# Kernel optimization log

Hardware: AMD Instinct MI355X
Metric: run time of the kernel (lower is better)

Reference implementation:

```python
import jax, jax.numpy as jnp
import numpy as np

NOTE_RES = 64  # global constant in the original repo; equals D of rep


def _down(x):
    # conv1d with kernel [0.5, 0.5], stride 2 over last axis (even length)
    return 0.5 * (x[..., ::2] + x[..., 1::2])


def setup_inputs() -> dict:
    key = jax.random.key(0)
    k1, k2, k3 = jax.random.split(key, 3)
    B, D, T = 32, NOTE_RES, 4096
    rep = jax.random.normal(k1, (B, D, T), dtype=jnp.float32)
    duration_mask = jax.random.uniform(k2, (B, D, T), dtype=jnp.float32)
    position_mask = jax.random.uniform(k3, (B, D, T), dtype=jnp.float32)
    return {
        "rep": rep,
        "duration_mask": duration_mask,
        "position_mask": position_mask,
        "low_duration": 1,
        "up_duration": 64,
    }


def reference(rep, duration_mask, position_mask, low_duration, up_duration):
    B, D, T = rep.shape  # D == NOTE_RES
    x = jnp.transpose(rep, (0, 2, 1))  # [B, T, NOTE_RES]; conv axis is last
    densed = _down(x)                  # [B, T, NOTE_RES//2]
    pot = NOTE_RES // 2
    res = jnp.zeros((B, T), dtype=rep.dtype)
    for i in range(0, NOTE_RES - low_duration):
        win_len = NOTE_RES - i - 1
        if win_len == pot:
            # descend one pyramid level
            x = densed
            densed = _down(x) if i < NOTE_RES - 2 else None
            d = x  # [B, T, win_len]
            pot //= 2
        else:
            pad_len = win_len - pot
            # mix fine-resolution prefix with coarse suffix -> length win_len
            d = jnp.concatenate([x[..., : 2 * pad_len], densed[..., pad_len:]], axis=-1)
        if win_len < up_duration:
            # sum_w d[b,t,w] * position_mask[b,w,t], gated by duration_mask[b,win_len-1,t]
            contrib = duration_mask[:, win_len - 1, :] * jnp.einsum(
                "btw,bwt->bt", d, position_mask[:, :win_len, :]
            )
            res = res + contrib
    return res[:, None, :]  # [B, 1, T]
```

## Files before the change

### kernel.cpp

```cpp
#include <hip/hip_runtime.h>


#define TT 4096

__device__ __forceinline__ void async_load16(const float* g, float* l) {
  __builtin_amdgcn_global_load_lds(
      (const __attribute__((address_space(1))) void*)g,
      (__attribute__((address_space(3))) void*)l, 16, 0, 0);
}

template <int K0>
__device__ __forceinline__ float roleK(const float* __restrict__ lrep,
                                       const float* __restrict__ lpm,
                                       const float* __restrict__ ldm, int lane,
                                       int low, int up) {
  constexpr int PADN = (K0 + 8 < 32) ? (K0 + 8) : 32;
  constexpr int PMN = (2 * K0 + 14 < 62 ? 2 * K0 + 14 : 62) - K0 + 1;
  float xa[8];
#pragma unroll
  for (int i = 0; i < 8; ++i)
    xa[i] = 0.5f * (lrep[(2 * (K0 + i)) * 64 + lane] +
                    lrep[(2 * (K0 + i) + 1) * 64 + lane]);
  float pmv[PMN];
#pragma unroll
  for (int r = 0; r < PMN; ++r) pmv[r] = lpm[(K0 + r) * 64 + lane];
  float res = 0.f;
#pragma unroll
  for (int pad = 0; pad < PADN; ++pad) {
    const int L = 32 + pad;
    const int kk0 = (pad > K0) ? pad : K0;
    float s = 0.f;
#pragma unroll
    for (int k = kk0; k < K0 + 8; ++k)
      s = fmaf(xa[k - K0], pmv[k + pad - K0], s);
    if (L >= low && L < up) res = fmaf(ldm[(31 + pad) * 64 + lane], s, res);
  }
  return res;
}

__device__ __forceinline__ float role3(const float* __restrict__ lrep,
                                       const float* __restrict__ lpm,
                                       const float* __restrict__ ldm, int lane,
                                       int low, int up) {
  float pmv[31];
#pragma unroll
  for (int r = 0; r < 31; ++r) pmv[r] = lpm[r * 64 + lane];
  float x1[32];
#pragma unroll
  for (int j = 0; j < 32; ++j)
    x1[j] = 0.5f * (lrep[(2 * j) * 64 + lane] + lrep[(2 * j + 1) * 64 + lane]);
  float res = 0.f;
#pragma unroll
  for (int pad = 0; pad < 8; ++pad) {
    const int L = 32 + pad;
    float s = 0.f;
#pragma unroll
    for (int k = pad; k < 8; ++k) s = fmaf(x1[k], pmv[k + pad], s);
    if (L >= low && L < up) res = fmaf(ldm[(31 + pad) * 64 + lane], s, res);
  }
  float x2[16], q1[16];
#pragma unroll
  for (int j = 0; j < 16; ++j) {
    const float a = x1[2 * j], b = x1[2 * j + 1];
    x2[j] = 0.5f * (a + b);
    q1[j] = a * pmv[2 * j] + b * pmv[2 * j + 1];
  }
  float p = 0.f;
#pragma unroll
  for (int pad = 0; pad < 16; ++pad) {
    const int L = 16 + pad;
    float s = p;
#pragma unroll
    for (int k = pad; k < 16; ++k) s = fmaf(x2[k], pmv[k + pad], s);
    if (L >= low && L < up) res = fmaf(ldm[(15 + pad) * 64 + lane], s, res);
    p += q1[pad];
  }
  return res;
}

__device__ __forceinline__ float role4(const float* __restrict__ lrep,
                                       const float* __restrict__ lpm,
                                       const float* __restrict__ ldm, int lane,
                                       int low, int up) {
  float res = 0.f, p = 0.f;
#pragma unroll
  for (int pad = 1; pad < 32; ++pad) {
    const int j = pad - 1;
    const float a = lrep[(2 * j) * 64 + lane];
    const float b = lrep[(2 * j + 1) * 64 + lane];
    const float pa = lpm[(2 * j) * 64 + lane];
    const float pb = lpm[(2 * j + 1) * 64 + lane];
    p = fmaf(a, pa, fmaf(b, pb, p));
    const int L = 32 + pad;
    if (L >= low && L < up) res = fmaf(ldm[(31 + pad) * 64 + lane], p, res);
  }
  return res;
}

template <int M>
__device__ __forceinline__ void level_step(const float* pmv,
                                           const float* __restrict__ ldm,
                                           int lane, int low, int up, float* xf,
                                           float* xc, float& res) {
  float q[M];
#pragma unroll
  for (int j = 0; j < M; ++j) {
    const float a = xf[2 * j], b = xf[2 * j + 1];
    xc[j] = 0.5f * (a + b);
    q[j] = a * pmv[2 * j] + b * pmv[2 * j + 1];
  }
  float p = 0.f;
#pragma unroll
  for (int pad = 0; pad < M; ++pad) {
    const int L = M + pad;
    float s = p;
#pragma unroll
    for (int k = pad; k < M; ++k) s = fmaf(xc[k], pmv[k + pad], s);
    if (L >= low && L < up) res = fmaf(ldm[(M - 1 + pad) * 64 + lane], s, res);
    p += q[pad];
  }
}

__device__ __forceinline__ float role5(const float* __restrict__ lrep,
                                       const float* __restrict__ lpm,
                                       const float* __restrict__ ldm, int lane,
                                       int low, int up) {
  float pmv[15];
#pragma unroll
  for (int r = 0; r < 15; ++r) pmv[r] = lpm[r * 64 + lane];
  float x1[32];
#pragma unroll
  for (int j = 0; j < 32; ++j)
    x1[j] = 0.5f * (lrep[(2 * j) * 64 + lane] + lrep[(2 * j + 1) * 64 + lane]);
  float x2[16];
#pragma unroll
  for (int j = 0; j < 16; ++j) x2[j] = 0.5f * (x1[2 * j] + x1[2 * j + 1]);
  float res = 0.f;
  float x3[8], x4[4], x5[2], x6[1];
  level_step<8>(pmv, ldm, lane, low, up, x2, x3, res);
  level_step<4>(pmv, ldm, lane, low, up, x3, x4, res);
  level_step<2>(pmv, ldm, lane, low, up, x4, x5, res);
  level_step<1>(pmv, ldm, lane, low, up, x5, x6, res);
  return res;
}

__global__ __launch_bounds__(384, 3) void ContextGenerator_34875134444049_kernel(
    const float* __restrict__ rep, const float* __restrict__ dm,
    const float* __restrict__ pm, const int* __restrict__ lowp,
    const int* __restrict__ upp, float* __restrict__ out) {
  __shared__ float lds[192 * 64 + 6 * 64];
  const int wid = threadIdx.x >> 6;
  const int lane = threadIdx.x & 63;
  const int b = blockIdx.x >> 6;
  const int t0 = (blockIdx.x & 63) << 6;
  const size_t base = (size_t)b * 64 * TT + (size_t)t0;

  const size_t lv = (size_t)(lane >> 4) * TT + (size_t)((lane & 15) << 2);
  for (int g = wid; g < 48; g += 6) {
    const float* tbase = (g < 16) ? rep + base
                       : (g < 32) ? pm + base - (size_t)64 * TT
                                  : dm + base - (size_t)128 * TT;
    const float* src = tbase + (size_t)(g << 2) * TT + lv;
    async_load16(src, &lds[g * 256]);
  }

  const int low = lowp[0];
  const int up = upp[0];

  __syncthreads();

  const float* lrep = lds;
  const float* lpm = lds + 64 * 64;
  const float* ldm = lds + 128 * 64;
  float* part = lds + 192 * 64;

  float res;
  if (wid == 0)
    res = roleK<24>(lrep, lpm, ldm, lane, low, up);
  else if (wid == 1)
    res = roleK<16>(lrep, lpm, ldm, lane, low, up);
  else if (wid == 2)
    res = roleK<8>(lrep, lpm, ldm, lane, low, up);
  else if (wid == 3)
    res = role3(lrep, lpm, ldm, lane, low, up);
  else if (wid == 4)
    res = role4(lrep, lpm, ldm, lane, low, up);
  else
    res = role5(lrep, lpm, ldm, lane, low, up);

  if (wid > 0) part[wid * 64 + lane] = res;
  __syncthreads();
  if (wid == 0)
    out[(size_t)b * TT + t0 + lane] = res + part[64 + lane] + part[128 + lane] +
                                      part[192 + lane] + part[256 + lane] +
                                      part[320 + lane];
}

extern "C" void kernel_launch(void* const* d_in, const int* in_sizes, int n_in,
                              void* d_out, int out_size, void* d_ws,
                              size_t ws_size, hipStream_t stream) {
  const float* rep = (const float*)d_in[0];
  const float* dm = (const float*)d_in[1];
  const float* pm = (const float*)d_in[2];
  const int* lowp = (const int*)d_in[3];
  const int* upp = (const int*)d_in[4];
  float* out = (float*)d_out;

  const int blocks = out_size / 64;
  ContextGenerator_34875134444049_kernel<<<blocks, 384, 0, stream>>>(
      rep, dm, pm, lowp, upp, out);
}
```

Measured before the change: 125.7 us.

## Process eight time chunks per block with double-buffered async LDS staging

```diff
diff --git a/kernel.cpp b/kernel.cpp
--- a/kernel.cpp
+++ b/kernel.cpp
@@ -2,11 +2,26 @@
 
 
 #define TT 4096
+#define SL (192 * 64)
 
 __device__ __forceinline__ void async_load16(const float* g, float* l) {
   __builtin_amdgcn_global_load_lds(
       (const __attribute__((address_space(1))) void*)g,
       (__attribute__((address_space(3))) void*)l, 16, 0, 0);
+}
+
+__device__ __forceinline__ void stage(const float* __restrict__ rep,
+                                      const float* __restrict__ dm,
+                                      const float* __restrict__ pm, size_t base,
+                                      float* buf, int wid, int lane) {
+  const size_t lv = (size_t)(lane >> 4) * TT + (size_t)((lane & 15) << 2);
+  for (int g = wid; g < 48; g += 6) {
+    const float* tbase = (g < 16) ? rep + base
+                       : (g < 32) ? pm + base - (size_t)64 * TT
+                                  : dm + base - (size_t)128 * TT;
+    const float* src = tbase + (size_t)(g << 2) * TT + lv;
+    async_load16(src, &buf[g * 256]);
+  }
 }
 
 template <int K0>
@@ -144,56 +159,53 @@
   return res;
 }
 
-__global__ __launch_bounds__(384, 3) void ContextGenerator_34875134444049_kernel(
+__device__ __forceinline__ float compute_role(const float* __restrict__ buf,
+                                              int wid, int lane, int low,
+                                              int up) {
+  const float* lrep = buf;
+  const float* lpm = buf + 64 * 64;
+  const float* ldm = buf + 128 * 64;
+  if (wid == 0) return roleK<24>(lrep, lpm, ldm, lane, low, up);
+  if (wid == 1) return roleK<16>(lrep, lpm, ldm, lane, low, up);
+  if (wid == 2) return roleK<8>(lrep, lpm, ldm, lane, low, up);
+  if (wid == 3) return role3(lrep, lpm, ldm, lane, low, up);
+  if (wid == 4) return role4(lrep, lpm, ldm, lane, low, up);
+  return role5(lrep, lpm, ldm, lane, low, up);
+}
+
+__global__ __launch_bounds__(384) void ContextGenerator_34875134444049_kernel(
     const float* __restrict__ rep, const float* __restrict__ dm,
     const float* __restrict__ pm, const int* __restrict__ lowp,
     const int* __restrict__ upp, float* __restrict__ out) {
-  __shared__ float lds[192 * 64 + 6 * 64];
+  __shared__ float lds[2 * SL + 6 * 64];
   const int wid = threadIdx.x >> 6;
   const int lane = threadIdx.x & 63;
-  const int b = blockIdx.x >> 6;
-  const int t0 = (blockIdx.x & 63) << 6;
-  const size_t base = (size_t)b * 64 * TT + (size_t)t0;
-
-  const size_t lv = (size_t)(lane >> 4) * TT + (size_t)((lane & 15) << 2);
-  for (int g = wid; g < 48; g += 6) {
-    const float* tbase = (g < 16) ? rep + base
-                       : (g < 32) ? pm + base - (size_t)64 * TT
-                                  : dm + base - (size_t)128 * TT;
-    const float* src = tbase + (size_t)(g << 2) * TT + lv;
-    async_load16(src, &lds[g * 256]);
-  }
+  const int b = blockIdx.x >> 3;
+  const int c0 = (blockIdx.x & 7) << 3;
+  const size_t bbase = (size_t)b * 64 * TT;
+  float* part = lds + 2 * SL;
 
   const int low = lowp[0];
   const int up = upp[0];
 
-  __syncthreads();
-
-  const float* lrep = lds;
-  const float* lpm = lds + 64 * 64;
-  const float* ldm = lds + 128 * 64;
-  float* part = lds + 192 * 64;
-
-  float res;
-  if (wid == 0)
-    res = roleK<24>(lrep, lpm, ldm, lane, low, up);
-  else if (wid == 1)
-    res = roleK<16>(lrep, lpm, ldm, lane, low, up);
-  else if (wid == 2)
-    res = roleK<8>(lrep, lpm, ldm, lane, low, up);
-  else if (wid == 3)
-    res = role3(lrep, lpm, ldm, lane, low, up);
-  else if (wid == 4)
-    res = role4(lrep, lpm, ldm, lane, low, up);
-  else
-    res = role5(lrep, lpm, ldm, lane, low, up);
-
-  if (wid > 0) part[wid * 64 + lane] = res;
-  __syncthreads();
-  if (wid == 0)
-    out[(size_t)b * TT + t0 + lane] = res + part[64 + lane] + part[128 + lane] +
-                                      part[192 + lane] + part[256 + lane] +
-                                      part[320 + lane];
+  stage(rep, dm, pm, bbase + ((size_t)c0 << 6), lds, wid, lane);
+
+#pragma unroll 1
+  for (int s = 0; s < 8; ++s) {
+    float* cur = lds + (s & 1) * SL;
+    float* nxt = lds + ((s + 1) & 1) * SL;
+    __syncthreads();
+    if (s < 7)
+      stage(rep, dm, pm, bbase + ((size_t)(c0 + s + 1) << 6), nxt, wid, lane);
+
+    const float res = compute_role(cur, wid, lane, low, up);
+    if (wid > 0) part[wid * 64 + lane] = res;
+    __syncthreads();
+    if (wid == 0)
+      out[(size_t)b * TT + ((size_t)(c0 + s) << 6) + lane] =
+          res + part[64 + lane] + part[128 + lane] + part[192 + lane] +
+          part[256 + lane] + part[320 + lane];
+  }
 }
 
 extern "C" void kernel_launch(void* const* d_in, const int* in_sizes, int n_in,
@@ -206,7 +218,7 @@
   const int* upp = (const int*)d_in[4];
   float* out = (float*)d_out;
 
-  const int blocks = out_size / 64;
+  const int blocks = out_size / 512;
   ContextGenerator_34875134444049_kernel<<<blocks, 384, 0, stream>>>(
       rep, dm, pm, lowp, upp, out);
 }
```

Result: no change. 128.0 us (+1.8%).

## Load duration mask directly to registers and stage rep/pm via register loads

Applied to the files above, without the earlier changes.

```diff
diff --git a/kernel.cpp b/kernel.cpp
--- a/kernel.cpp
+++ b/kernel.cpp
@@ -2,28 +2,18 @@
 
 
 #define TT 4096
-
-__device__ __forceinline__ void async_load16(const float* g, float* l) {
-  __builtin_amdgcn_global_load_lds(
-      (const __attribute__((address_space(1))) void*)g,
-      (__attribute__((address_space(3))) void*)l, 16, 0, 0);
-}
 
 template <int K0>
 __device__ __forceinline__ float roleK(const float* __restrict__ lrep,
                                        const float* __restrict__ lpm,
-                                       const float* __restrict__ ldm, int lane,
-                                       int low, int up) {
+                                       const float* dmv, int lane, int low,
+                                       int up) {
   constexpr int PADN = (K0 + 8 < 32) ? (K0 + 8) : 32;
-  constexpr int PMN = (2 * K0 + 14 < 62 ? 2 * K0 + 14 : 62) - K0 + 1;
   float xa[8];
 #pragma unroll
   for (int i = 0; i < 8; ++i)
     xa[i] = 0.5f * (lrep[(2 * (K0 + i)) * 64 + lane] +
                     lrep[(2 * (K0 + i) + 1) * 64 + lane]);
-  float pmv[PMN];
-#pragma unroll
-  for (int r = 0; r < PMN; ++r) pmv[r] = lpm[(K0 + r) * 64 + lane];
   float res = 0.f;
 #pragma unroll
   for (int pad = 0; pad < PADN; ++pad) {
@@ -32,19 +22,16 @@
     float s = 0.f;
 #pragma unroll
     for (int k = kk0; k < K0 + 8; ++k)
-      s = fmaf(xa[k - K0], pmv[k + pad - K0], s);
-    if (L >= low && L < up) res = fmaf(ldm[(31 + pad) * 64 + lane], s, res);
+      s = fmaf(xa[k - K0], lpm[(k + pad) * 64 + lane], s);
+    if (L >= low && L < up) res = fmaf(dmv[pad], s, res);
   }
   return res;
 }
 
 __device__ __forceinline__ float role3(const float* __restrict__ lrep,
                                        const float* __restrict__ lpm,
-                                       const float* __restrict__ ldm, int lane,
-                                       int low, int up) {
-  float pmv[31];
-#pragma unroll
-  for (int r = 0; r < 31; ++r) pmv[r] = lpm[r * 64 + lane];
+                                       const float* dmv, int lane, int low,
+                                       int up) {
   float x1[32];
 #pragma unroll
   for (int j = 0; j < 32; ++j)
@@ -55,15 +42,15 @@
     const int L = 32 + pad;
     float s = 0.f;
 #pragma unroll
-    for (int k = pad; k < 8; ++k) s = fmaf(x1[k], pmv[k + pad], s);
-    if (L >= low && L < up) res = fmaf(ldm[(31 + pad) * 64 + lane], s, res);
+    for (int k = pad; k < 8; ++k) s = fmaf(x1[k], lpm[(k + pad) * 64 + lane], s);
+    if (L >= low && L < up) res = fmaf(dmv[16 + pad], s, res);
   }
   float x2[16], q1[16];
 #pragma unroll
   for (int j = 0; j < 16; ++j) {
-    const float a = x1[2 * j], b = x1[2 * j + 1];
-    x2[j] = 0.5f * (a + b);
-    q1[j] = a * pmv[2 * j] + b * pmv[2 * j + 1];
+    const float a = x1[2 * j], bb = x1[2 * j + 1];
+    x2[j] = 0.5f * (a + bb);
+    q1[j] = a * lpm[(2 * j) * 64 + lane] + bb * lpm[(2 * j + 1) * 64 + lane];
   }
   float p = 0.f;
 #pragma unroll
@@ -71,8 +58,8 @@
     const int L = 16 + pad;
     float s = p;
 #pragma unroll
-    for (int k = pad; k < 16; ++k) s = fmaf(x2[k], pmv[k + pad], s);
-    if (L >= low && L < up) res = fmaf(ldm[(15 + pad) * 64 + lane], s, res);
+    for (int k = pad; k < 16; ++k) s = fmaf(x2[k], lpm[(k + pad) * 64 + lane], s);
+    if (L >= low && L < up) res = fmaf(dmv[pad], s, res);
     p += q1[pad];
   }
   return res;
@@ -80,34 +67,32 @@
 
 __device__ __forceinline__ float role4(const float* __restrict__ lrep,
                                        const float* __restrict__ lpm,
-                                       const float* __restrict__ ldm, int lane,
-                                       int low, int up) {
+                                       const float* dmv, int lane, int low,
+                                       int up) {
   float res = 0.f, p = 0.f;
 #pragma unroll
   for (int pad = 1; pad < 32; ++pad) {
     const int j = pad - 1;
-    const float a = lrep[(2 * j) * 64 + lane];
-    const float b = lrep[(2 * j + 1) * 64 + lane];
-    const float pa = lpm[(2 * j) * 64 + lane];
-    const float pb = lpm[(2 * j + 1) * 64 + lane];
-    p = fmaf(a, pa, fmaf(b, pb, p));
+    p = fmaf(lrep[(2 * j) * 64 + lane], lpm[(2 * j) * 64 + lane],
+             fmaf(lrep[(2 * j + 1) * 64 + lane], lpm[(2 * j + 1) * 64 + lane],
+                  p));
     const int L = 32 + pad;
-    if (L >= low && L < up) res = fmaf(ldm[(31 + pad) * 64 + lane], p, res);
+    if (L >= low && L < up) res = fmaf(dmv[pad - 1], p, res);
   }
   return res;
 }
 
 template <int M>
-__device__ __forceinline__ void level_step(const float* pmv,
-                                           const float* __restrict__ ldm,
-                                           int lane, int low, int up, float* xf,
-                                           float* xc, float& res) {
+__device__ __forceinline__ void level_step(const float* __restrict__ lpm,
+                                           const float* dmv, int lane, int low,
+                                           int up, float* xf, float* xc,
+                                           float& res) {
   float q[M];
 #pragma unroll
   for (int j = 0; j < M; ++j) {
-    const float a = xf[2 * j], b = xf[2 * j + 1];
-    xc[j] = 0.5f * (a + b);
-    q[j] = a * pmv[2 * j] + b * pmv[2 * j + 1];
+    const float a = xf[2 * j], bb = xf[2 * j + 1];
+    xc[j] = 0.5f * (a + bb);
+    q[j] = a * lpm[(2 * j) * 64 + lane] + bb * lpm[(2 * j + 1) * 64 + lane];
   }
   float p = 0.f;
 #pragma unroll
@@ -115,19 +100,16 @@
     const int L = M + pad;
     float s = p;
 #pragma unroll
-    for (int k = pad; k < M; ++k) s = fmaf(xc[k], pmv[k + pad], s);
-    if (L >= low && L < up) res = fmaf(ldm[(M - 1 + pad) * 64 + lane], s, res);
+    for (int k = pad; k < M; ++k) s = fmaf(xc[k], lpm[(k + pad) * 64 + lane], s);
+    if (L >= low && L < up) res = fmaf(dmv[M - 1 + pad], s, res);
     p += q[pad];
   }
 }
 
 __device__ __forceinline__ float role5(const float* __restrict__ lrep,
                                        const float* __restrict__ lpm,
-                                       const float* __restrict__ ldm, int lane,
-                                       int low, int up) {
-  float pmv[15];
-#pragma unroll
-  for (int r = 0; r < 15; ++r) pmv[r] = lpm[r * 64 + lane];
+                                       const float* dmv, int lane, int low,
+                                       int up) {
   float x1[32];
 #pragma unroll
   for (int j = 0; j < 32; ++j)
@@ -137,56 +119,85 @@
   for (int j = 0; j < 16; ++j) x2[j] = 0.5f * (x1[2 * j] + x1[2 * j + 1]);
   float res = 0.f;
   float x3[8], x4[4], x5[2], x6[1];
-  level_step<8>(pmv, ldm, lane, low, up, x2, x3, res);
-  level_step<4>(pmv, ldm, lane, low, up, x3, x4, res);
-  level_step<2>(pmv, ldm, lane, low, up, x4, x5, res);
-  level_step<1>(pmv, ldm, lane, low, up, x5, x6, res);
-  return res;
-}
-
-__global__ __launch_bounds__(384, 3) void ContextGenerator_34875134444049_kernel(
+  level_step<8>(lpm, dmv, lane, low, up, x2, x3, res);
+  level_step<4>(lpm, dmv, lane, low, up, x3, x4, res);
+  level_step<2>(lpm, dmv, lane, low, up, x4, x5, res);
+  level_step<1>(lpm, dmv, lane, low, up, x5, x6, res);
+  return res;
+}
+
+__global__ __launch_bounds__(384) void ContextGenerator_34875134444049_kernel(
     const float* __restrict__ rep, const float* __restrict__ dm,
     const float* __restrict__ pm, const int* __restrict__ lowp,
     const int* __restrict__ upp, float* __restrict__ out) {
-  __shared__ float lds[192 * 64 + 6 * 64];
-  const int wid = threadIdx.x >> 6;
-  const int lane = threadIdx.x & 63;
+  __shared__ float lds[128 * 64 + 6 * 64];
+  const int tid = threadIdx.x;
+  const int wid = tid >> 6;
+  const int lane = tid & 63;
   const int b = blockIdx.x >> 6;
   const int t0 = (blockIdx.x & 63) << 6;
   const size_t base = (size_t)b * 64 * TT + (size_t)t0;
 
-  const size_t lv = (size_t)(lane >> 4) * TT + (size_t)((lane & 15) << 2);
-  for (int g = wid; g < 48; g += 6) {
-    const float* tbase = (g < 16) ? rep + base
-                       : (g < 32) ? pm + base - (size_t)64 * TT
-                                  : dm + base - (size_t)128 * TT;
-    const float* src = tbase + (size_t)(g << 2) * TT + lv;
-    async_load16(src, &lds[g * 256]);
+  const int rcol = (tid & 15) << 2;
+  float4 v[6];
+#pragma unroll
+  for (int g = 0; g < 6; ++g) {
+    const int row = (tid >> 4) + 24 * g;
+    if (row < 128) {
+      const float* tb = (row < 64) ? rep + base + (size_t)row * TT
+                                   : pm + base + (size_t)(row - 64) * TT;
+      v[g] = *(const float4*)(tb + rcol);
+    }
   }
 
   const int low = lowp[0];
   const int up = upp[0];
-
+  const float* dmg = dm + base + lane;
+  float dmv[32];
+  if (wid == 0) {
+#pragma unroll
+    for (int i = 0; i < 32; ++i) dmv[i] = dmg[(size_t)(31 + i) * TT];
+  } else if (wid == 1) {
+#pragma unroll
+    for (int i = 0; i < 24; ++i) dmv[i] = dmg[(size_t)(31 + i) * TT];
+  } else if (wid == 2) {
+#pragma unroll
+    for (int i = 0; i < 16; ++i) dmv[i] = dmg[(size_t)(31 + i) * TT];
+  } else if (wid == 3) {
+#pragma unroll
+    for (int i = 0; i < 24; ++i) dmv[i] = dmg[(size_t)(15 + i) * TT];
+  } else if (wid == 4) {
+#pragma unroll
+    for (int i = 0; i < 31; ++i) dmv[i] = dmg[(size_t)(32 + i) * TT];
+  } else {
+#pragma unroll
+    for (int i = 0; i < 15; ++i) dmv[i] = dmg[(size_t)i * TT];
+  }
+
+#pragma unroll
+  for (int g = 0; g < 6; ++g) {
+    const int row = (tid >> 4) + 24 * g;
+    if (row < 128) *(float4*)(&lds[row * 64 + rcol]) = v[g];
+  }
   __syncthreads();
 
   const float* lrep = lds;
   const float* lpm = lds + 64 * 64;
-  const float* ldm = lds + 128 * 64;
-  float* part = lds + 192 * 64;
+  float* part = lds + 128 * 64;
 
   float res;
   if (wid == 0)
-    res = roleK<24>(lrep, lpm, ldm, lane, low, up);
+    res = roleK<24>(lrep, lpm, dmv, lane, low, up);
   else if (wid == 1)
-    res = roleK<16>(lrep, lpm, ldm, lane, low, up);
+    res = roleK<16>(lrep, lpm, dmv, lane, low, up);
   else if (wid == 2)
-    res = roleK<8>(lrep, lpm, ldm, lane, low, up);
+    res = roleK<8>(lrep, lpm, dmv, lane, low, up);
   else if (wid == 3)
-    res = role3(lrep, lpm, ldm, lane, low, up);
+    res = role3(lrep, lpm, dmv, lane, low, up);
   else if (wid == 4)
-    res = role4(lrep, lpm, ldm, lane, low, up);
+    res = role4(lrep, lpm, dmv, lane, low, up);
   else
-    res = role5(lrep, lpm, ldm, lane, low, up);
+    res = role5(lrep, lpm, dmv, lane, low, up);
 
   if (wid > 0) part[wid * 64 + lane] = res;
   __syncthreads();
```

Result: slower. 156.1 us (+24.2%).
